# Optimization experiments

Measured on AMD Instinct MI355X. Metric: run time of the kernel, lower is better.

Reference implementation:

```python
import jax, jax.numpy as jnp
import numpy as np

N_NODES = 50000
N_EDGES = 640000
DIM_IN = 128
DIM_OUT = 64
NUM_GRAPHS = 512


def gcn_conv(x, W, b, src, dst, n_nodes):
    # GCNConv with add_self_loops=True, symmetric normalization.
    h = x @ W                                   # [N, d]
    ones = jnp.ones((src.shape[0],), h.dtype)
    deg = 1.0 + jax.ops.segment_sum(ones, dst, num_segments=n_nodes)  # self-loop included
    dinv = jax.lax.rsqrt(deg)                   # [N]
    coef = dinv[src] * dinv[dst]                # [E]
    agg = jax.ops.segment_sum(h[src] * coef[:, None], dst, num_segments=n_nodes)
    # self-loop contribution: dinv[i]^2 * h[i]
    return agg + h * (dinv * dinv)[:, None] + b


def setup_inputs() -> dict:
    key = jax.random.key(0)
    ks = jax.random.split(key, 8)
    x = jax.random.normal(ks[0], (N_NODES, DIM_IN), dtype=jnp.float32)
    edge_index = jax.random.randint(ks[1], (2, N_EDGES), 0, N_NODES, dtype=jnp.int32)
    x_batch = jnp.sort(jax.random.randint(ks[2], (N_NODES,), 0, NUM_GRAPHS, dtype=jnp.int32))
    s = 1.0 / np.sqrt(DIM_IN)
    W1 = jax.random.uniform(ks[3], (DIM_IN, DIM_IN), jnp.float32, -s, s)
    b1 = jnp.zeros((DIM_IN,), jnp.float32)
    W2 = jax.random.uniform(ks[4], (DIM_IN, DIM_IN), jnp.float32, -s, s)
    b2 = jnp.zeros((DIM_IN,), jnp.float32)
    Wh = jax.random.uniform(ks[5], (DIM_IN, DIM_OUT), jnp.float32, -s, s)
    bh = jnp.zeros((DIM_OUT,), jnp.float32)
    return {"x": x, "edge_index": edge_index, "x_batch": x_batch,
            "W1": W1, "b1": b1, "W2": W2, "b2": b2, "Wh": Wh, "bh": bh}


def reference(x, edge_index, x_batch, W1, b1, W2, b2, Wh, bh):
    src, dst = edge_index[0], edge_index[1]
    n = x.shape[0]
    # layer 1: GCNConv + relu (dropout is identity in eval mode)
    h = jax.nn.relu(gcn_conv(x, W1, b1, src, dst, n))
    # layer 2
    h = jax.nn.relu(gcn_conv(h, W2, b2, src, dst, n))
    # global_add_pool over graph ids
    pooled = jax.ops.segment_sum(h, x_batch, num_segments=NUM_GRAPHS)  # [G, d]
    logits = pooled @ Wh + bh                                          # [G, C]
    return jax.nn.log_softmax(logits, axis=1)
```

## Files before the change

### kernel.cpp

```cpp
#include <hip/hip_runtime.h>
#include <hip/hip_bf16.h>


#define DIM 128
#define NCLS 64
#define SLOTS 64
#define POISON 0xAAAAAAAAu
#define HROWS 65536

typedef __attribute__((ext_vector_type(8))) short bf16x8;
typedef __attribute__((ext_vector_type(8))) unsigned short u16x8;
typedef __attribute__((ext_vector_type(4))) float floatx4;

__device__ inline float b2f(unsigned short u) {
    union { unsigned int i; float f; } v; v.i = ((unsigned int)u) << 16; return v.f;
}
__device__ inline unsigned short f2b(float f) {
    union { float f; unsigned int i; } v; v.f = f;
    unsigned int r = v.i + 0x7FFFu + ((v.i >> 16) & 1u);
    return (unsigned short)(r >> 16);
}
__device__ inline float deg_to_dinv(int cnt_raw) {
    return rsqrtf(1.0f + (float)(int)((unsigned)cnt_raw - POISON));
}


__global__ __launch_bounds__(256) void prep_all(const float* __restrict__ W1,
                                                const float* __restrict__ W2,
                                                unsigned short* __restrict__ O1,
                                                unsigned short* __restrict__ O2,
                                                const int* __restrict__ src,
                                                const int* __restrict__ dst,
                                                int* __restrict__ cnt,
                                                unsigned short* __restrict__ slot,
                                                int N, int E) {
    const int gtid = blockIdx.x * 256 + threadIdx.x;
    const int gs = gridDim.x * 256;

    for (int idx = gtid; idx < 2 * DIM * DIM; idx += gs) {
        int which = idx >> 14;
        int id2 = idx & (DIM * DIM - 1);
        const float* W = which ? W2 : W1;
        unsigned short* O = which ? O2 : O1;
        int k = id2 >> 7, nn = id2 & 127;
        int ntile = nn >> 4, k0i = k >> 5;
        int ln = ((k >> 3) & 3) * 16 + (nn & 15);
        int j = k & 7;
        O[(((ntile * 4 + k0i) * 64) + ln) * 8 + j] = f2b(W[id2]);
    }

    const int grp = blockIdx.x & 7;
    const int npg = (N + 7) >> 3;
    const int lo = grp * npg;
    const int hi = (lo + npg < N) ? (lo + npg) : N;
    const int sb = (blockIdx.x >> 3) * 256 + threadIdx.x;
    const int ss = (gridDim.x >> 3) * 256;
    const int ne4 = E >> 2;
    for (int e4 = sb; e4 < ne4; e4 += ss) {
        int4 s = ((const int4*)src)[e4];
        int4 d = ((const int4*)dst)[e4];
        if (d.x >= lo && d.x < hi) {
            unsigned p = (unsigned)atomicAdd(&cnt[d.x], 1) - POISON;
            if (p < SLOTS) slot[d.x * SLOTS + p] = (unsigned short)s.x;
        }
        if (d.y >= lo && d.y < hi) {
            unsigned p = (unsigned)atomicAdd(&cnt[d.y], 1) - POISON;
            if (p < SLOTS) slot[d.y * SLOTS + p] = (unsigned short)s.y;
        }
        if (d.z >= lo && d.z < hi) {
            unsigned p = (unsigned)atomicAdd(&cnt[d.z], 1) - POISON;
            if (p < SLOTS) slot[d.z * SLOTS + p] = (unsigned short)s.z;
        }
        if (d.w >= lo && d.w < hi) {
            unsigned p = (unsigned)atomicAdd(&cnt[d.w], 1) - POISON;
            if (p < SLOTS) slot[d.w * SLOTS + p] = (unsigned short)s.w;
        }
    }
    if (sb == 0) {
        for (int e = ne4 * 4; e < E; ++e) {
            int d = dst[e];
            if (d >= lo && d < hi) {
                unsigned p = (unsigned)atomicAdd(&cnt[d], 1) - POISON;
                if (p < SLOTS) slot[d * SLOTS + p] = (unsigned short)src[e];
            }
        }
    }
}


__global__ __launch_bounds__(256) void gemm1(const float* __restrict__ A,
                                             const unsigned short* __restrict__ Wswz,
                                             unsigned short* __restrict__ C,
                                             const int* __restrict__ cnt, int N) {
    const int wave = threadIdx.x >> 6;
    const int lane = threadIdx.x & 63;
    const int quad = lane >> 4;
    const int l16 = lane & 15;
    const int row0 = blockIdx.x * 64 + wave * 16;
    const int r = row0 + l16;
    const int rc = (r < N) ? r : (N - 1);
    const float di = deg_to_dinv(cnt[rc]);

    bf16x8 a[4];
    #pragma unroll
    for (int k0i = 0; k0i < 4; ++k0i) {
        int k = k0i * 32 + quad * 8;
        const float4* p = (const float4*)(A + (long)rc * DIM + k);
        float4 f0 = p[0], f1 = p[1];
        bf16x8 t;
        t[0] = (short)f2b(f0.x * di); t[1] = (short)f2b(f0.y * di);
        t[2] = (short)f2b(f0.z * di); t[3] = (short)f2b(f0.w * di);
        t[4] = (short)f2b(f1.x * di); t[5] = (short)f2b(f1.y * di);
        t[6] = (short)f2b(f1.z * di); t[7] = (short)f2b(f1.w * di);
        a[k0i] = t;
    }

    #pragma unroll
    for (int ntile = 0; ntile < 8; ++ntile) {
        floatx4 acc = {0.f, 0.f, 0.f, 0.f};
        #pragma unroll
        for (int k0i = 0; k0i < 4; ++k0i) {
            bf16x8 b = *(const bf16x8*)(Wswz + (((ntile * 4 + k0i) * 64) + lane) * 8);
            acc = __builtin_amdgcn_mfma_f32_16x16x32_bf16(a[k0i], b, acc, 0, 0, 0);
        }
        #pragma unroll
        for (int reg = 0; reg < 4; ++reg) {
            int rr = row0 + quad * 4 + reg;
            if (rr < N) C[(long)rr * DIM + ntile * 16 + l16] = f2b(acc[reg]);
        }
    }
}


__device__ inline void agg4(const ushort2* __restrict__ h,
                            const int* __restrict__ cnt,
                            const unsigned short* __restrict__ slot,
                            int i0, int c2, float bx, float by, int N,
                            float2 res[4]) {
    int deg[4]; float di[4]; float ax[4], ay[4]; int ro[4];
    #pragma unroll
    for (int q = 0; q < 4; ++q) {
        int ii = i0 + q;
        int ic = (ii < N) ? ii : 0;
        int d = (int)((unsigned)cnt[ic] - POISON);
        deg[q] = (ii < N) ? (d < SLOTS ? d : SLOTS) : 0;
        di[q] = rsqrtf(1.0f + (float)d);
        ushort2 hv = h[ic * 64 + c2];
        ax[q] = b2f(hv.x);
        ay[q] = b2f(hv.y);
        ro[q] = ic * SLOTS;
    }
    int mx = max(max(deg[0], deg[1]), max(deg[2], deg[3]));
    for (int e = 0; e < mx; e += 8) {
        u16x8 qa[4];
        #pragma unroll
        for (int q = 0; q < 4; ++q)
            qa[q] = *(const u16x8*)(slot + ro[q] + e);
        ushort2 hv[4][8];
        #pragma unroll
        for (int q = 0; q < 4; ++q)
            #pragma unroll
            for (int k = 0; k < 8; ++k)
                hv[q][k] = h[(int)qa[q][k] * 64 + c2];
        #pragma unroll
        for (int q = 0; q < 4; ++q)
            #pragma unroll
            for (int k = 0; k < 8; ++k) {
                ax[q] += b2f(hv[q][k].x);
                ay[q] += b2f(hv[q][k].y);
            }
    }
    #pragma unroll
    for (int q = 0; q < 4; ++q) {
        res[q].x = fmaxf(fmaf(di[q], ax[q], bx), 0.f);
        res[q].y = fmaxf(fmaf(di[q], ay[q], by), 0.f);
    }
}


__global__ __launch_bounds__(256) void agg_gemm(const ushort2* __restrict__ h,
                                                const int* __restrict__ cnt,
                                                const unsigned short* __restrict__ slot,
                                                const float* __restrict__ bias,
                                                const unsigned short* __restrict__ Wswz,
                                                unsigned short* __restrict__ C, int N) {
    __shared__ unsigned short As[16 * 136];
    const int wv = threadIdx.x >> 6;
    const int c2 = threadIdx.x & 63;
    const int tile0 = blockIdx.x * 16;
    const float bx = bias[2 * c2], by = bias[2 * c2 + 1];

    float2 res[4];
    agg4(h, cnt, slot, tile0 + wv * 4, c2, bx, by, N, res);
    #pragma unroll
    for (int q = 0; q < 4; ++q) {
        int r = wv * 4 + q;
        ushort2 o; o.x = f2b(res[q].x); o.y = f2b(res[q].y);
        *(ushort2*)(&As[r * 136 + 2 * c2]) = o;
    }
    __syncthreads();

    const int lane = threadIdx.x & 63;
    const int quad = lane >> 4;
    const int l16 = lane & 15;
    bf16x8 a[4];
    #pragma unroll
    for (int k0i = 0; k0i < 4; ++k0i)
        a[k0i] = *(const bf16x8*)(&As[l16 * 136 + k0i * 32 + quad * 8]);

    float dro[4];
    #pragma unroll
    for (int reg = 0; reg < 4; ++reg) {
        int rr = tile0 + quad * 4 + reg;
        dro[reg] = deg_to_dinv(cnt[(rr < N) ? rr : 0]);
    }

    #pragma unroll
    for (int nt = 0; nt < 2; ++nt) {
        int ntile = wv * 2 + nt;
        floatx4 acc = {0.f, 0.f, 0.f, 0.f};
        #pragma unroll
        for (int k0i = 0; k0i < 4; ++k0i) {
            bf16x8 b = *(const bf16x8*)(Wswz + (((ntile * 4 + k0i) * 64) + lane) * 8);
            acc = __builtin_amdgcn_mfma_f32_16x16x32_bf16(a[k0i], b, acc, 0, 0, 0);
        }
        #pragma unroll
        for (int reg = 0; reg < 4; ++reg) {
            int rr = tile0 + quad * 4 + reg;
            if (rr < N) C[(long)rr * DIM + ntile * 16 + l16] = f2b(acc[reg] * dro[reg]);
        }
    }
}


__global__ __launch_bounds__(256) void agg_pool(const ushort2* __restrict__ h,
                                                const int* __restrict__ cnt,
                                                const unsigned short* __restrict__ slot,
                                                const float* __restrict__ bias,
                                                const int* __restrict__ xb,
                                                float* __restrict__ pooled, int N) {
    const int wv = threadIdx.x >> 6;
    const int c2 = threadIdx.x & 63;
    const int tile0 = blockIdx.x * 16;
    const float bx = bias[2 * c2], by = bias[2 * c2 + 1];

    float2 res[4];
    agg4(h, cnt, slot, tile0 + wv * 4, c2, bx, by, N, res);

    int gcur = -1;
    float gx = 0.f, gy = 0.f;
    #pragma unroll
    for (int q = 0; q < 4; ++q) {
        int i = tile0 + wv * 4 + q;
        if (i >= N) break;
        int g = xb[i];
        if (g != gcur) {
            if (gcur >= 0) {
                atomicAdd(&pooled[gcur * DIM + 2 * c2], gx);
                atomicAdd(&pooled[gcur * DIM + 2 * c2 + 1], gy);
            }
            gcur = g; gx = 0.f; gy = 0.f;
        }
        gx += res[q].x; gy += res[q].y;
    }
    if (gcur >= 0) {
        atomicAdd(&pooled[gcur * DIM + 2 * c2], gx);
        atomicAdd(&pooled[gcur * DIM + 2 * c2 + 1], gy);
    }
}


__global__ __launch_bounds__(256) void head(const float* __restrict__ pooled,
                                            const float* __restrict__ Wh,
                                            const float* __restrict__ bh,
                                            float* __restrict__ out, int G) {
    int g = blockIdx.x * 4 + (threadIdx.x >> 6);
    if (g >= G) return;
    int o = threadIdx.x & 63;
    float logit = bh[o];
    #pragma unroll 8
    for (int c = 0; c < DIM; ++c)
        logit = fmaf(pooled[g * DIM + c], Wh[c * NCLS + o], logit);
    float m = logit;
    #pragma unroll
    for (int d = 32; d >= 1; d >>= 1) m = fmaxf(m, __shfl_xor(m, d, 64));
    float ex = __expf(logit - m);
    float ssum = ex;
    #pragma unroll
    for (int d = 32; d >= 1; d >>= 1) ssum += __shfl_xor(ssum, d, 64);
    out[g * NCLS + o] = logit - m - __logf(ssum);
}


extern "C" void kernel_launch(void* const* d_in, const int* in_sizes, int n_in,
                              void* d_out, int out_size, void* d_ws, size_t ws_size,
                              hipStream_t stream) {
    const float* x  = (const float*)d_in[0];
    const int*   ei = (const int*)d_in[1];
    const int*   xb = (const int*)d_in[2];
    const float* W1 = (const float*)d_in[3];
    const float* b1 = (const float*)d_in[4];
    const float* W2 = (const float*)d_in[5];
    const float* b2 = (const float*)d_in[6];
    const float* Wh = (const float*)d_in[7];
    const float* bh = (const float*)d_in[8];
    float* out = (float*)d_out;

    const int N = in_sizes[0] / DIM;
    const int E = in_sizes[1] / 2;
    const int G = out_size / NCLS;
    const int* srcv = ei;
    const int* dstv = ei + E;

    char* w = (char*)d_ws;
    auto alloc = [&](size_t bytes) {
        char* p = w;
        w += (bytes + 255) & ~(size_t)255;
        return p;
    };
    int* cnt = (int*)alloc((size_t)N * 4);
    unsigned short* slot = (unsigned short*)alloc((size_t)N * SLOTS * 2);
    unsigned short* Wswz1 = (unsigned short*)alloc((size_t)DIM * DIM * 2);
    unsigned short* Wswz2 = (unsigned short*)alloc((size_t)DIM * DIM * 2);
    unsigned short* Htmp  = (unsigned short*)alloc((size_t)HROWS * DIM * 2);
    unsigned short* Htmp2 = (unsigned short*)alloc((size_t)HROWS * DIM * 2);
    float* pooled = (float*)alloc((size_t)G * DIM * 4);

    hipMemsetAsync(slot, 0xFF, (size_t)N * SLOTS * 2, stream);

    prep_all<<<1024, 256, 0, stream>>>(W1, W2, Wswz1, Wswz2, srcv, dstv,
                                       cnt, slot, N, E);
    gemm1<<<(N + 63) / 64, 256, 0, stream>>>(x, Wswz1, Htmp, cnt, N);
    agg_gemm<<<(N + 15) / 16, 256, 0, stream>>>((const ushort2*)Htmp, cnt, slot,
                                                b1, Wswz2, Htmp2, N);
    agg_pool<<<(N + 15) / 16, 256, 0, stream>>>((const ushort2*)Htmp2, cnt, slot,
                                                b2, xb, pooled, N);
    head<<<(G + 3) / 4, 256, 0, stream>>>(pooled, Wh, bh, out, G);
}
```

Before: 190.2 us.

## Store hidden features as FP8 split into column halves for gather aggregation

Intermediate node features are now written as FP8 instead of bf16 and stored in two 64-column halves. Each half is aggregated by its own kernel pass so the gathered working set is smaller and more cache-friendly. The fused aggregate-then-GEMM kernel is split into an aggregation store plus a separate GEMM, which adds extra launches and a bf16 round trip through memory. FP8 storage loses precision compared with bf16 and may affect accuracy.

```diff
diff --git a/kernel.cpp b/kernel.cpp
--- a/kernel.cpp
+++ b/kernel.cpp
@@ -3,6 +3,7 @@
 
 
 #define DIM 128
+#define HALF 64
 #define NCLS 64
 #define SLOTS 64
 #define POISON 0xAAAAAAAAu
@@ -19,6 +20,10 @@
     union { float f; unsigned int i; } v; v.f = f;
     unsigned int r = v.i + 0x7FFFu + ((v.i >> 16) & 1u);
     return (unsigned short)(r >> 16);
+}
+__device__ inline unsigned char f2fp8(float f) {
+    int pk = __builtin_amdgcn_cvt_pk_fp8_f32(f, f, 0, false);
+    return (unsigned char)(pk & 0xFF);
 }
 __device__ inline float deg_to_dinv(int cnt_raw) {
     return rsqrtf(1.0f + (float)(int)((unsigned)cnt_raw - POISON));
@@ -33,9 +38,18 @@
                                                 const int* __restrict__ dst,
                                                 int* __restrict__ cnt,
                                                 unsigned short* __restrict__ slot,
+                                                unsigned char* __restrict__ h1lo,
+                                                unsigned char* __restrict__ h1hi,
+                                                unsigned char* __restrict__ h2lo,
+                                                unsigned char* __restrict__ h2hi,
                                                 int N, int E) {
     const int gtid = blockIdx.x * 256 + threadIdx.x;
     const int gs = gridDim.x * 256;
+
+    if (gtid < 16)      ((int*)(h1lo + (size_t)0xFFFF * HALF))[gtid] = 0;
+    else if (gtid < 32) ((int*)(h1hi + (size_t)0xFFFF * HALF))[gtid - 16] = 0;
+    else if (gtid < 48) ((int*)(h2lo + (size_t)0xFFFF * HALF))[gtid - 32] = 0;
+    else if (gtid < 64) ((int*)(h2hi + (size_t)0xFFFF * HALF))[gtid - 48] = 0;
 
     for (int idx = gtid; idx < 2 * DIM * DIM; idx += gs) {
         int which = idx >> 14;
@@ -90,7 +104,8 @@
 
 __global__ __launch_bounds__(256) void gemm1(const float* __restrict__ A,
                                              const unsigned short* __restrict__ Wswz,
-                                             unsigned short* __restrict__ C,
+                                             unsigned char* __restrict__ Clo,
+                                             unsigned char* __restrict__ Chi,
                                              const int* __restrict__ cnt, int N) {
     const int wave = threadIdx.x >> 6;
     const int lane = threadIdx.x & 63;
@@ -126,98 +141,126 @@
         #pragma unroll
         for (int reg = 0; reg < 4; ++reg) {
             int rr = row0 + quad * 4 + reg;
-            if (rr < N) C[(long)rr * DIM + ntile * 16 + l16] = f2b(acc[reg]);
-        }
-    }
-}
-
-
-__device__ inline void agg4(const ushort2* __restrict__ h,
-                            const int* __restrict__ cnt,
-                            const unsigned short* __restrict__ slot,
-                            int i0, int c2, float bx, float by, int N,
-                            float2 res[4]) {
-    int deg[4]; float di[4]; float ax[4], ay[4]; int ro[4];
-    #pragma unroll
-    for (int q = 0; q < 4; ++q) {
-        int ii = i0 + q;
-        int ic = (ii < N) ? ii : 0;
-        int d = (int)((unsigned)cnt[ic] - POISON);
-        deg[q] = (ii < N) ? (d < SLOTS ? d : SLOTS) : 0;
-        di[q] = rsqrtf(1.0f + (float)d);
-        ushort2 hv = h[ic * 64 + c2];
-        ax[q] = b2f(hv.x);
-        ay[q] = b2f(hv.y);
-        ro[q] = ic * SLOTS;
-    }
-    int mx = max(max(deg[0], deg[1]), max(deg[2], deg[3]));
-    for (int e = 0; e < mx; e += 8) {
-        u16x8 qa[4];
-        #pragma unroll
-        for (int q = 0; q < 4; ++q)
-            qa[q] = *(const u16x8*)(slot + ro[q] + e);
-        ushort2 hv[4][8];
-        #pragma unroll
-        for (int q = 0; q < 4; ++q)
-            #pragma unroll
-            for (int k = 0; k < 8; ++k)
-                hv[q][k] = h[(int)qa[q][k] * 64 + c2];
-        #pragma unroll
-        for (int q = 0; q < 4; ++q)
-            #pragma unroll
-            for (int k = 0; k < 8; ++k) {
-                ax[q] += b2f(hv[q][k].x);
-                ay[q] += b2f(hv[q][k].y);
+            if (rr < N) {
+                unsigned char v = f2fp8(acc[reg]);
+                if (ntile < 4) Clo[(long)rr * HALF + ntile * 16 + l16] = v;
+                else           Chi[(long)rr * HALF + (ntile - 4) * 16 + l16] = v;
             }
-    }
-    #pragma unroll
-    for (int q = 0; q < 4; ++q) {
-        res[q].x = fmaxf(fmaf(di[q], ax[q], bx), 0.f);
-        res[q].y = fmaxf(fmaf(di[q], ay[q], by), 0.f);
-    }
-}
-
-
-__global__ __launch_bounds__(256) void agg_gemm(const ushort2* __restrict__ h,
-                                                const int* __restrict__ cnt,
-                                                const unsigned short* __restrict__ slot,
-                                                const float* __restrict__ bias,
-                                                const unsigned short* __restrict__ Wswz,
-                                                unsigned short* __restrict__ C, int N) {
-    __shared__ unsigned short As[16 * 136];
+        }
+    }
+}
+
+
+__device__ inline void agg4h(const unsigned short* __restrict__ h,
+                             const int* __restrict__ cnt,
+                             const unsigned short* __restrict__ slot,
+                             const float* __restrict__ bias, int hoff,
+                             int i0, int lane, int N, float2 res[2]) {
+    const int sub = lane >> 5;
+    const int cc = lane & 31;
+    const int n0 = i0 + sub, n1 = i0 + sub + 2;
+    const int ic0 = (n0 < N) ? n0 : 0;
+    const int ic1 = (n1 < N) ? n1 : 0;
+    const int d0 = (int)((unsigned)cnt[ic0] - POISON);
+    const int d1 = (int)((unsigned)cnt[ic1] - POISON);
+    const int deg0 = (n0 < N) ? (d0 < SLOTS ? d0 : SLOTS) : 0;
+    const int deg1 = (n1 < N) ? (d1 < SLOTS ? d1 : SLOTS) : 0;
+    const float di0 = rsqrtf(1.0f + (float)d0);
+    const float di1 = rsqrtf(1.0f + (float)d1);
+
+    unsigned short w0 = h[ic0 * 32 + cc];
+    unsigned short w1 = h[ic1 * 32 + cc];
+    float a0x = __builtin_amdgcn_cvt_f32_fp8(w0, 0);
+    float a0y = __builtin_amdgcn_cvt_f32_fp8(w0, 1);
+    float a1x = __builtin_amdgcn_cvt_f32_fp8(w1, 0);
+    float a1y = __builtin_amdgcn_cvt_f32_fp8(w1, 1);
+
+    int m = (deg0 > deg1) ? deg0 : deg1;
+    m = max(m, __shfl_xor(m, 32, 64));
+
+    const int ro0 = ic0 * SLOTS, ro1 = ic1 * SLOTS;
+    for (int e = 0; e < m; e += 8) {
+        u16x8 qa0 = __builtin_nontemporal_load((const u16x8*)(slot + ro0 + e));
+        u16x8 qa1 = __builtin_nontemporal_load((const u16x8*)(slot + ro1 + e));
+        unsigned short hv0[8], hv1[8];
+        #pragma unroll
+        for (int k = 0; k < 8; ++k) hv0[k] = h[(int)qa0[k] * 32 + cc];
+        #pragma unroll
+        for (int k = 0; k < 8; ++k) hv1[k] = h[(int)qa1[k] * 32 + cc];
+        #pragma unroll
+        for (int k = 0; k < 8; ++k) {
+            a0x += __builtin_amdgcn_cvt_f32_fp8(hv0[k], 0);
+            a0y += __builtin_amdgcn_cvt_f32_fp8(hv0[k], 1);
+            a1x += __builtin_amdgcn_cvt_f32_fp8(hv1[k], 0);
+            a1y += __builtin_amdgcn_cvt_f32_fp8(hv1[k], 1);
+        }
+    }
+
+    const float2 b = *(const float2*)(bias + hoff + 2 * cc);
+    res[0].x = fmaxf(fmaf(di0, a0x, b.x), 0.f);
+    res[0].y = fmaxf(fmaf(di0, a0y, b.y), 0.f);
+    res[1].x = fmaxf(fmaf(di1, a1x, b.x), 0.f);
+    res[1].y = fmaxf(fmaf(di1, a1y, b.y), 0.f);
+}
+
+
+__global__ __launch_bounds__(256) void agg_store(const unsigned short* __restrict__ h,
+                                                 const int* __restrict__ cnt,
+                                                 const unsigned short* __restrict__ slot,
+                                                 const float* __restrict__ bias, int hoff,
+                                                 unsigned short* __restrict__ Agg, int N) {
     const int wv = threadIdx.x >> 6;
-    const int c2 = threadIdx.x & 63;
-    const int tile0 = blockIdx.x * 16;
-    const float bx = bias[2 * c2], by = bias[2 * c2 + 1];
-
-    float2 res[4];
-    agg4(h, cnt, slot, tile0 + wv * 4, c2, bx, by, N, res);
-    #pragma unroll
-    for (int q = 0; q < 4; ++q) {
-        int r = wv * 4 + q;
-        ushort2 o; o.x = f2b(res[q].x); o.y = f2b(res[q].y);
-        *(ushort2*)(&As[r * 136 + 2 * c2]) = o;
-    }
-    __syncthreads();
-
+    const int lane = threadIdx.x & 63;
+    const int i0 = blockIdx.x * 16 + wv * 4;
+
+    float2 res[2];
+    agg4h(h, cnt, slot, bias, hoff, i0, lane, N, res);
+
+    const int sub = lane >> 5;
+    const int cc = lane & 31;
+    const int n0 = i0 + sub, n1 = i0 + sub + 2;
+    if (n0 < N) {
+        unsigned v = (unsigned)f2b(res[0].x) | ((unsigned)f2b(res[0].y) << 16);
+        __builtin_nontemporal_store(v, (unsigned*)(Agg + (long)n0 * HALF + 2 * cc));
+    }
+    if (n1 < N) {
+        unsigned v = (unsigned)f2b(res[1].x) | ((unsigned)f2b(res[1].y) << 16);
+        __builtin_nontemporal_store(v, (unsigned*)(Agg + (long)n1 * HALF + 2 * cc));
+    }
+}
+
+
+__global__ __launch_bounds__(256) void gemm2(const unsigned short* __restrict__ Alo,
+                                             const unsigned short* __restrict__ Ahi,
+                                             const unsigned short* __restrict__ Wswz,
+                                             unsigned char* __restrict__ Clo,
+                                             unsigned char* __restrict__ Chi,
+                                             const int* __restrict__ cnt, int N) {
+    const int wave = threadIdx.x >> 6;
     const int lane = threadIdx.x & 63;
     const int quad = lane >> 4;
     const int l16 = lane & 15;
+    const int row0 = blockIdx.x * 64 + wave * 16;
+    const int r = row0 + l16;
+    const int rc = (r < N) ? r : (N - 1);
+
     bf16x8 a[4];
     #pragma unroll
-    for (int k0i = 0; k0i < 4; ++k0i)
-        a[k0i] = *(const bf16x8*)(&As[l16 * 136 + k0i * 32 + quad * 8]);
+    for (int k0i = 0; k0i < 4; ++k0i) {
+        int koff = (k0i & 1) * 32 + quad * 8;
+        const unsigned short* src = (k0i < 2) ? Alo : Ahi;
+        a[k0i] = *(const bf16x8*)(src + (long)rc * HALF + koff);
+    }
 
     float dro[4];
     #pragma unroll
     for (int reg = 0; reg < 4; ++reg) {
-        int rr = tile0 + quad * 4 + reg;
+        int rr = row0 + quad * 4 + reg;
         dro[reg] = deg_to_dinv(cnt[(rr < N) ? rr : 0]);
     }
 
     #pragma unroll
-    for (int nt = 0; nt < 2; ++nt) {
-        int ntile = wv * 2 + nt;
+    for (int ntile = 0; ntile < 8; ++ntile) {
         floatx4 acc = {0.f, 0.f, 0.f, 0.f};
         #pragma unroll
         for (int k0i = 0; k0i < 4; ++k0i) {
@@ -226,46 +269,49 @@
         }
         #pragma unroll
         for (int reg = 0; reg < 4; ++reg) {
-            int rr = tile0 + quad * 4 + reg;
-            if (rr < N) C[(long)rr * DIM + ntile * 16 + l16] = f2b(acc[reg] * dro[reg]);
-        }
-    }
-}
-
-
-__global__ __launch_bounds__(256) void agg_pool(const ushort2* __restrict__ h,
-                                                const int* __restrict__ cnt,
-                                                const unsigned short* __restrict__ slot,
-                                                const float* __restrict__ bias,
-                                                const int* __restrict__ xb,
-                                                float* __restrict__ pooled, int N) {
+            int rr = row0 + quad * 4 + reg;
+            if (rr < N) {
+                unsigned char v = f2fp8(acc[reg] * dro[reg]);
+                if (ntile < 4) Clo[(long)rr * HALF + ntile * 16 + l16] = v;
+                else           Chi[(long)rr * HALF + (ntile - 4) * 16 + l16] = v;
+            }
+        }
+    }
+}
+
+
+__global__ __launch_bounds__(256) void agg_pool2(const unsigned short* __restrict__ h,
+                                                 const int* __restrict__ cnt,
+                                                 const unsigned short* __restrict__ slot,
+                                                 const float* __restrict__ bias, int hoff,
+                                                 const int* __restrict__ xb,
+                                                 float* __restrict__ pooled, int N) {
     const int wv = threadIdx.x >> 6;
-    const int c2 = threadIdx.x & 63;
-    const int tile0 = blockIdx.x * 16;
-    const float bx = bias[2 * c2], by = bias[2 * c2 + 1];
-
-    float2 res[4];
-    agg4(h, cnt, slot, tile0 + wv * 4, c2, bx, by, N, res);
-
-    int gcur = -1;
-    float gx = 0.f, gy = 0.f;
-    #pragma unroll
-    for (int q = 0; q < 4; ++q) {
-        int i = tile0 + wv * 4 + q;
-        if (i >= N) break;
-        int g = xb[i];
-        if (g != gcur) {
-            if (gcur >= 0) {
-                atomicAdd(&pooled[gcur * DIM + 2 * c2], gx);
-                atomicAdd(&pooled[gcur * DIM + 2 * c2 + 1], gy);
-            }
-            gcur = g; gx = 0.f; gy = 0.f;
-        }
-        gx += res[q].x; gy += res[q].y;
-    }
-    if (gcur >= 0) {
-        atomicAdd(&pooled[gcur * DIM + 2 * c2], gx);
-        atomicAdd(&pooled[gcur * DIM + 2 * c2 + 1], gy);
+    const int lane = threadIdx.x & 63;
+    const int i0 = blockIdx.x * 16 + wv * 4;
+
+    float2 res[2];
+    agg4h(h, cnt, slot, bias, hoff, i0, lane, N, res);
+
+    const int sub = lane >> 5;
+    const int cc = lane & 31;
+    const int n0 = i0 + sub, n1 = i0 + sub + 2;
+    const bool v0 = n0 < N, v1 = n1 < N;
+    const int g0 = xb[v0 ? n0 : 0];
+    const int g1 = xb[v1 ? n1 : 0];
+    float* base = pooled + hoff + 2 * cc;
+    if (v0 && v1 && g0 == g1) {
+        atomicAdd(base + (long)g0 * DIM,     res[0].x + res[1].x);
+        atomicAdd(base + (long)g0 * DIM + 1, res[0].y + res[1].y);
+    } else {
+        if (v0) {
+            atomicAdd(base + (long)g0 * DIM,     res[0].x);
+            atomicAdd(base + (long)g0 * DIM + 1, res[0].y);
+        }
+        if (v1) {
+            atomicAdd(base + (long)g1 * DIM,     res[1].x);
+            atomicAdd(base + (long)g1 * DIM + 1, res[1].y);
+        }
     }
 }
 
@@ -322,18 +368,28 @@
     unsigned short* slot = (unsigned short*)alloc((size_t)N * SLOTS * 2);
     unsigned short* Wswz1 = (unsigned short*)alloc((size_t)DIM * DIM * 2);
     unsigned short* Wswz2 = (unsigned short*)alloc((size_t)DIM * DIM * 2);
-    unsigned short* Htmp  = (unsigned short*)alloc((size_t)HROWS * DIM * 2);
-    unsigned short* Htmp2 = (unsigned short*)alloc((size_t)HROWS * DIM * 2);
+    unsigned char* H1lo = (unsigned char*)alloc((size_t)HROWS * HALF);
+    unsigned char* H1hi = (unsigned char*)alloc((size_t)HROWS * HALF);
+    unsigned char* H2lo = (unsigned char*)alloc((size_t)HROWS * HALF);
+    unsigned char* H2hi = (unsigned char*)alloc((size_t)HROWS * HALF);
+    unsigned short* Agg1lo = (unsigned short*)alloc((size_t)N * HALF * 2);
+    unsigned short* Agg1hi = (unsigned short*)alloc((size_t)N * HALF * 2);
     float* pooled = (float*)alloc((size_t)G * DIM * 4);
 
     hipMemsetAsync(slot, 0xFF, (size_t)N * SLOTS * 2, stream);
 
     prep_all<<<1024, 256, 0, stream>>>(W1, W2, Wswz1, Wswz2, srcv, dstv,
-                                       cnt, slot, N, E);
-    gemm1<<<(N + 63) / 64, 256, 0, stream>>>(x, Wswz1, Htmp, cnt, N);
-    agg_gemm<<<(N + 15) / 16, 256, 0, stream>>>((const ushort2*)Htmp, cnt, slot,
-                                                b1, Wswz2, Htmp2, N);
-    agg_pool<<<(N + 15) / 16, 256, 0, stream>>>((const ushort2*)Htmp2, cnt, slot,
-                                                b2, xb, pooled, N);
+                                       cnt, slot, H1lo, H1hi, H2lo, H2hi, N, E);
+    gemm1<<<(N + 63) / 64, 256, 0, stream>>>(x, Wswz1, H1lo, H1hi, cnt, N);
+    agg_store<<<(N + 15) / 16, 256, 0, stream>>>((const unsigned short*)H1lo, cnt,
+                                                 slot, b1, 0, Agg1lo, N);
+    agg_store<<<(N + 15) / 16, 256, 0, stream>>>((const unsigned short*)H1hi, cnt,
+                                                 slot, b1, HALF, Agg1hi, N);
+    gemm2<<<(N + 63) / 64, 256, 0, stream>>>(Agg1lo, Agg1hi, Wswz2,
+                                             H2lo, H2hi, cnt, N);
+    agg_pool2<<<(N + 15) / 16, 256, 0, stream>>>((const unsigned short*)H2lo, cnt,
+                                                 slot, b2, 0, xb, pooled, N);
+    agg_pool2<<<(N + 15) / 16, 256, 0, stream>>>((const unsigned short*)H2hi, cnt,
+                                                 slot, b2, HALF, xb, pooled, N);
     head<<<(G + 3) / 4, 256, 0, stream>>>(pooled, Wh, bh, out, G);
 }
```

Result: slower. 223.8 us (+17.7%).
